# Kernel tuning notes

Measured on AMD Instinct MI355X. Metric: run time of the kernel, lower is better.

## Reference

```python
import jax, jax.numpy as jnp
from jax import lax
import numpy as np

B, S = 4096, 200           # batch, max history length
MAX_LEN, STEP = 1024, 4    # module init args
BINS = MAX_LEN // STEP     # 256 time bins
H = 64                     # LSTM hidden (dimension)


def setup_inputs() -> dict:
    key = jax.random.key(0)
    ks = jax.random.split(key, 8)
    time = jax.random.uniform(ks[0], (B, S), jnp.float32, 0.0, 1000.0)
    # predict_time >= max event time per row (module assumes nonnegative bin index)
    predict_time = jnp.max(time, axis=1) + jax.random.uniform(ks[1], (B,), jnp.float32, 0.0, 24.0)
    length = jax.random.randint(ks[2], (B,), 1, S + 1, jnp.int32)
    # torch nn.LSTM init: uniform(-1/sqrt(H), 1/sqrt(H)); gate order i,f,g,o
    s = 1.0 / np.sqrt(H)
    W_ih = jax.random.uniform(ks[3], (4 * H, 1), jnp.float32, -s, s)
    W_hh = jax.random.uniform(ks[4], (4 * H, H), jnp.float32, -s, s)
    b_ih = jax.random.uniform(ks[5], (4 * H,), jnp.float32, -s, s)
    b_hh = jax.random.uniform(ks[6], (4 * H,), jnp.float32, -s, s)
    return {"time": time, "length": length, "predict_time": predict_time,
            "W_ih": W_ih, "W_hh": W_hh, "b_ih": b_ih, "b_hh": b_hh}


def _histogram(time, length, predict_time):
    # pos = int((predict_time - time_ij) / STEP), incremented at bin BINS-1-pos
    pos = ((predict_time[:, None] - time) / STEP).astype(jnp.int32)  # trunc toward 0, like int()
    valid = (jnp.arange(S)[None, :] < length[:, None]) & (pos >= 0) & (pos < BINS)
    idx = BINS - 1 - jnp.clip(pos, 0, BINS - 1)
    hist = jnp.zeros((B, BINS), jnp.float32)
    hist = hist.at[jnp.arange(B)[:, None], idx].add(valid.astype(jnp.float32))
    return hist  # [B, BINS]


def _lstm_final_h(x, W_ih, W_hh, b_ih, b_hh):
    # x: [B, T] scalar sequence (input_size=1). Returns final hidden state [B, H].
    b = b_ih + b_hh

    def step(carry, x_t):
        h, c = carry
        gates = x_t[:, None] * W_ih[:, 0][None, :] + h @ W_hh.T + b  # [B, 4H]
        i, f, g, o = jnp.split(gates, 4, axis=1)
        c = jax.nn.sigmoid(f) * c + jax.nn.sigmoid(i) * jnp.tanh(g)
        h = jax.nn.sigmoid(o) * jnp.tanh(c)
        return (h, c), None

    init = (jnp.zeros((B, H), x.dtype), jnp.zeros((B, H), x.dtype))
    (h, _), _ = lax.scan(step, init, jnp.moveaxis(x, 1, 0))  # scan over T
    return h


def reference(time, length, predict_time, W_ih, W_hh, b_ih, b_hh):
    hist = _histogram(time, length, predict_time)
    return _lstm_final_h(hist, W_ih, W_hh, b_ih, b_hh)
```

## Files before the change

### kernel.cpp

```cpp
#include <hip/hip_runtime.h>
#include <hip/hip_bf16.h>


#define B_S     200
#define B_T     256
#define ROWS    8
#define THREADS 256
#define HS      72
#define LOG2E   1.4426950408889634f

typedef __attribute__((ext_vector_type(8))) _Float16 half8;
typedef __attribute__((ext_vector_type(4))) float float4_t;

__device__ __forceinline__ float load_f(const void* p, int i, int isb) {
    if (isb) {
        unsigned short u = ((const unsigned short*)p)[i];
        return __uint_as_float(((unsigned int)u) << 16);
    }
    return ((const float*)p)[i];
}

__device__ __forceinline__ float act_one(float gi, float gf, float gg,
                                         float go, float& c) {
    float A  = __builtin_amdgcn_exp2f(gi);
    float F  = __builtin_amdgcn_exp2f(gf);
    float Bv = __builtin_amdgcn_exp2f(gg);
    float t1    = (1.0f + A) * (Bv + 1.0f);
    float oneF  = 1.0f + F;
    float numer = fmaf(c, t1, oneF * (Bv - 1.0f));
    float denom = oneF * t1;
    c = numer * __builtin_amdgcn_rcpf(denom);
    float D  = __builtin_amdgcn_exp2f(go);
    float cs = fminf(c * (2.0f * LOG2E), 126.0f);
    float E  = __builtin_amdgcn_exp2f(cs);
    return (E - 1.0f) * __builtin_amdgcn_rcpf((1.0f + D) * (E + 1.0f));
}

__global__ __launch_bounds__(THREADS, 2)
void trend_encoder_kernel(const void* __restrict__ time_,
                          const int*  __restrict__ length,
                          const void* __restrict__ ptime_,
                          const void* __restrict__ wih_,
                          const void* __restrict__ whh_,
                          const void* __restrict__ bih_,
                          const void* __restrict__ bhh_,
                          void* __restrict__ out_) {
    __shared__ __align__(16) float x_t[B_T * ROWS];
    __shared__ __align__(16) _Float16 h_sh[2][ROWS * HS];
    __shared__ int flag_sh;

    const int tid  = threadIdx.x;
    const int wv   = tid >> 6;
    const int lane = tid & 63;
    const int m    = lane & 15;
    const int quad = lane >> 4;
    const int b0   = blockIdx.x * ROWS;

    if (tid < 64) {
        unsigned short u = ((const unsigned short*)wih_)[tid];
        float v = __uint_as_float(((unsigned int)u) << 16);
        int bad = !(v > -0.2f && v < 0.2f);
        unsigned long long bm = __ballot(bad);
        if (lane == 0) flag_sh = (bm == 0ULL) ? 1 : 0;
    }
    for (int i = tid; i < B_T * ROWS; i += THREADS) x_t[i] = 0.0f;
    for (int i = tid; i < 2 * ROWS * HS; i += THREADS)
        ((_Float16*)h_sh)[i] = (_Float16)0.0f;
    __syncthreads();
    const int isb = flag_sh;

    for (int e = tid; e < ROWS * B_S; e += THREADS) {
        int row  = e / B_S;
        int s    = e - row * B_S;
        int grow = b0 + row;
        if (s < length[grow]) {
            float pt = load_f(ptime_, grow, isb);
            float tv = load_f(time_, grow * B_S + s, isb);
            int pos = (int)((pt - tv) * 0.25f);
            if (pos >= 0 && pos < B_T)
                atomicAdd(&x_t[(B_T - 1 - pos) * ROWS + row], 1.0f);
        }
    }

    const float gsc[4] = {-LOG2E, -LOG2E, 2.0f * LOG2E, -LOG2E};
    half8 bw[4][2];
    float wihv[4], biasv[4];
    #pragma unroll
    for (int tt = 0; tt < 4; ++tt) {
        int n = 16 * wv + 64 * tt + m;
        float s = gsc[tt];
        wihv[tt]  = load_f(wih_, n, isb) * s;
        biasv[tt] = (load_f(bih_, n, isb) + load_f(bhh_, n, isb)) * s;
        #pragma unroll
        for (int c = 0; c < 2; ++c) {
            half8 v;
            #pragma unroll
            for (int j = 0; j < 8; ++j)
                v[j] = (_Float16)(load_f(whh_, n * 64 + 32 * c + 8 * quad + j, isb) * s);
            bw[tt][c] = v;
        }
    }

    const int aoff = (m & 7) * HS + 8 * quad;
    const int kcol = 16 * wv + m;
    const int lr0  = (quad & 1) * 4 + (quad >> 1) * 2;
    const int xq   = (quad & 1) * 4;
    const bool loq = (quad < 2);
    float c2[2] = {0.f, 0.f};
    float h2[2] = {0.f, 0.f};
    __syncthreads();

    for (int t = 0; t < B_T; ++t) {
        const int p = t & 1;
        const _Float16* hh = h_sh[p];
        half8 a0 = *(const half8*)&hh[aoff];
        half8 a1 = *(const half8*)&hh[aoff + 32];
        float4_t xv = *(const float4_t*)&x_t[t * ROWS + xq];

        float4_t acc[4];
        #pragma unroll
        for (int tt = 0; tt < 4; ++tt) {
            float4_t c;
            #pragma unroll
            for (int r = 0; r < 4; ++r) c[r] = fmaf(xv[r], wihv[tt], biasv[tt]);
            c = __builtin_amdgcn_mfma_f32_16x16x32_f16(a0, bw[tt][0], c, 0, 0, 0);
            c = __builtin_amdgcn_mfma_f32_16x16x32_f16(a1, bw[tt][1], c, 0, 0, 0);
            acc[tt] = c;
        }

        _Float16* wb = h_sh[p ^ 1];
        #pragma unroll
        for (int k = 0; k < 2; ++k) {
            float gi = loq ? acc[0][k] : acc[0][2 + k];
            float gf = loq ? acc[1][k] : acc[1][2 + k];
            float gg = loq ? acc[2][k] : acc[2][2 + k];
            float go = loq ? acc[3][k] : acc[3][2 + k];
            h2[k] = act_one(gi, gf, gg, go, c2[k]);
            wb[(lr0 + k) * HS + kcol] = (_Float16)h2[k];
        }
        __syncthreads();
    }

    #pragma unroll
    for (int k = 0; k < 2; ++k) {
        int o = (b0 + lr0 + k) * 64 + kcol;
        if (isb) ((__hip_bfloat16*)out_)[o] = __float2bfloat16(h2[k]);
        else     ((float*)out_)[o] = h2[k];
    }
}

extern "C" void kernel_launch(void* const* d_in, const int* in_sizes, int n_in,
                              void* d_out, int out_size, void* d_ws, size_t ws_size,
                              hipStream_t stream) {
    const void* time_  = d_in[0];
    const int*  length = (const int*)d_in[1];
    const void* ptime  = d_in[2];
    const void* wih    = d_in[3];
    const void* whh    = d_in[4];
    const void* bih    = d_in[5];
    const void* bhh    = d_in[6];

    const int B = in_sizes[1];
    trend_encoder_kernel<<<dim3(B / ROWS), dim3(THREADS), 0, stream>>>(
        time_, length, ptime, wih, whh, bih, bhh, d_out);
}
```

Baseline: 204.5 us.

## Give each wave independent batch rows to drop per-step block barriers

The recurrent loop is restructured so each wave owns 4 batch rows and computes all 256 gate columns for them. Its hidden state lives in a wave-private LDS slice, which removes the per-timestep __syncthreads and the double-buffered shared h. Rows per block double to 16, halving the grid, and the two-blocks-per-CU launch bound is dropped. In exchange each wave issues four times as many MFMAs per step, because A rows are replicated 4x to fill the 16-row tile. Each gate-column group's activation is computed right after its MFMAs, so work becomes serialized within a wave.

```diff
diff --git a/kernel.cpp b/kernel.cpp
--- a/kernel.cpp
+++ b/kernel.cpp
@@ -4,7 +4,7 @@
 
 #define B_S     200
 #define B_T     256
-#define ROWS    8
+#define ROWS    16
 #define THREADS 256
 #define HS      72
 #define LOG2E   1.4426950408889634f
@@ -36,7 +36,7 @@
     return (E - 1.0f) * __builtin_amdgcn_rcpf((1.0f + D) * (E + 1.0f));
 }
 
-__global__ __launch_bounds__(THREADS, 2)
+__global__ __launch_bounds__(THREADS)
 void trend_encoder_kernel(const void* __restrict__ time_,
                           const int*  __restrict__ length,
                           const void* __restrict__ ptime_,
@@ -46,14 +46,14 @@
                           const void* __restrict__ bhh_,
                           void* __restrict__ out_) {
     __shared__ __align__(16) float x_t[B_T * ROWS];
-    __shared__ __align__(16) _Float16 h_sh[2][ROWS * HS];
+    __shared__ __align__(16) _Float16 h_sh[4][4 * HS];
     __shared__ int flag_sh;
 
     const int tid  = threadIdx.x;
     const int wv   = tid >> 6;
     const int lane = tid & 63;
     const int m    = lane & 15;
-    const int quad = lane >> 4;
+    const int q    = lane >> 4;
     const int b0   = blockIdx.x * ROWS;
 
     if (tid < 64) {
@@ -64,7 +64,7 @@
         if (lane == 0) flag_sh = (bm == 0ULL) ? 1 : 0;
     }
     for (int i = tid; i < B_T * ROWS; i += THREADS) x_t[i] = 0.0f;
-    for (int i = tid; i < 2 * ROWS * HS; i += THREADS)
+    for (int i = tid; i < 4 * 4 * HS; i += THREADS)
         ((_Float16*)h_sh)[i] = (_Float16)0.0f;
     __syncthreads();
     const int isb = flag_sh;
@@ -83,69 +83,68 @@
     }
 
     const float gsc[4] = {-LOG2E, -LOG2E, 2.0f * LOG2E, -LOG2E};
-    half8 bw[4][2];
-    float wihv[4], biasv[4];
+    half8 bw[4][4][2];
+    float wihv[4][4], biasv[4][4];
     #pragma unroll
-    for (int tt = 0; tt < 4; ++tt) {
-        int n = 16 * wv + 64 * tt + m;
-        float s = gsc[tt];
-        wihv[tt]  = load_f(wih_, n, isb) * s;
-        biasv[tt] = (load_f(bih_, n, isb) + load_f(bhh_, n, isb)) * s;
+    for (int g = 0; g < 4; ++g) {
+        float s = gsc[g];
         #pragma unroll
-        for (int c = 0; c < 2; ++c) {
-            half8 v;
+        for (int cg = 0; cg < 4; ++cg) {
+            int n = 64 * g + 16 * cg + m;
+            wihv[g][cg]  = load_f(wih_, n, isb) * s;
+            biasv[g][cg] = (load_f(bih_, n, isb) + load_f(bhh_, n, isb)) * s;
             #pragma unroll
-            for (int j = 0; j < 8; ++j)
-                v[j] = (_Float16)(load_f(whh_, n * 64 + 32 * c + 8 * quad + j, isb) * s);
-            bw[tt][c] = v;
+            for (int c = 0; c < 2; ++c) {
+                half8 v;
+                #pragma unroll
+                for (int j = 0; j < 8; ++j)
+                    v[j] = (_Float16)(load_f(whh_, n * 64 + 32 * c + 8 * q + j, isb) * s);
+                bw[g][cg][c] = v;
+            }
         }
     }
 
-    const int aoff = (m & 7) * HS + 8 * quad;
-    const int kcol = 16 * wv + m;
-    const int lr0  = (quad & 1) * 4 + (quad >> 1) * 2;
-    const int xq   = (quad & 1) * 4;
-    const bool loq = (quad < 2);
-    float c2[2] = {0.f, 0.f};
-    float h2[2] = {0.f, 0.f};
+    const int arow = m >> 2;
+    const int aoff = arow * HS + 8 * q;
+    _Float16* hw = h_sh[wv];
+
+    float c4[4] = {0.f, 0.f, 0.f, 0.f};
+    float h4[4] = {0.f, 0.f, 0.f, 0.f};
+    float4_t acc[4][4];
+    #pragma unroll
+    for (int g = 0; g < 4; ++g)
+        #pragma unroll
+        for (int cg = 0; cg < 4; ++cg)
+            acc[g][cg] = (float4_t){0.f, 0.f, 0.f, 0.f};
+
     __syncthreads();
 
     for (int t = 0; t < B_T; ++t) {
-        const int p = t & 1;
-        const _Float16* hh = h_sh[p];
-        half8 a0 = *(const half8*)&hh[aoff];
-        half8 a1 = *(const half8*)&hh[aoff + 32];
-        float4_t xv = *(const float4_t*)&x_t[t * ROWS + xq];
+        float xq = x_t[t * ROWS + 4 * wv + q];
+        half8 a0 = *(const half8*)&hw[aoff];
+        half8 a1 = *(const half8*)&hw[aoff + 32];
 
-        float4_t acc[4];
         #pragma unroll
-        for (int tt = 0; tt < 4; ++tt) {
-            float4_t c;
+        for (int cg = 0; cg < 4; ++cg) {
             #pragma unroll
-            for (int r = 0; r < 4; ++r) c[r] = fmaf(xv[r], wihv[tt], biasv[tt]);
-            c = __builtin_amdgcn_mfma_f32_16x16x32_f16(a0, bw[tt][0], c, 0, 0, 0);
-            c = __builtin_amdgcn_mfma_f32_16x16x32_f16(a1, bw[tt][1], c, 0, 0, 0);
-            acc[tt] = c;
+            for (int g = 0; g < 4; ++g) {
+                acc[g][cg][0] = fmaf(xq, wihv[g][cg], biasv[g][cg]);
+                acc[g][cg] = __builtin_amdgcn_mfma_f32_16x16x32_f16(
+                                 a0, bw[g][cg][0], acc[g][cg], 0, 0, 0);
+                acc[g][cg] = __builtin_amdgcn_mfma_f32_16x16x32_f16(
+                                 a1, bw[g][cg][1], acc[g][cg], 0, 0, 0);
+            }
+            h4[cg] = act_one(acc[0][cg][0], acc[1][cg][0],
+                             acc[2][cg][0], acc[3][cg][0], c4[cg]);
+            hw[q * HS + 16 * cg + m] = (_Float16)h4[cg];
         }
-
-        _Float16* wb = h_sh[p ^ 1];
-        #pragma unroll
-        for (int k = 0; k < 2; ++k) {
-            float gi = loq ? acc[0][k] : acc[0][2 + k];
-            float gf = loq ? acc[1][k] : acc[1][2 + k];
-            float gg = loq ? acc[2][k] : acc[2][2 + k];
-            float go = loq ? acc[3][k] : acc[3][2 + k];
-            h2[k] = act_one(gi, gf, gg, go, c2[k]);
-            wb[(lr0 + k) * HS + kcol] = (_Float16)h2[k];
-        }
-        __syncthreads();
     }
 
     #pragma unroll
-    for (int k = 0; k < 2; ++k) {
-        int o = (b0 + lr0 + k) * 64 + kcol;
-        if (isb) ((__hip_bfloat16*)out_)[o] = __float2bfloat16(h2[k]);
-        else     ((float*)out_)[o] = h2[k];
+    for (int cg = 0; cg < 4; ++cg) {
+        int o = (b0 + 4 * wv + q) * 64 + 16 * cg + m;
+        if (isb) ((__hip_bfloat16*)out_)[o] = __float2bfloat16(h4[cg]);
+        else     ((float*)out_)[o] = h4[cg];
     }
 }
 
```

New measurement: 257.4 us. 25.9% more time.
